# Performance work log

Measured on AMD Instinct MI355X. Metric: run time of the kernel, lower is better.

Reference implementation:

```python
import jax, jax.numpy as jnp
import numpy as np
import math

D_MODEL = 1024
D_K = 256
B, T = 4, 4096

def setup_inputs() -> dict:
    key = jax.random.key(0)
    ks = jax.random.split(key, 7)
    s = 1.0 / math.sqrt(D_MODEL)
    return {
        "inputs": jax.random.normal(ks[0], (B, T, D_MODEL), dtype=jnp.float32),
        "Wq": jax.random.uniform(ks[1], (D_MODEL, D_K), jnp.float32, -s, s),
        "bq": jax.random.uniform(ks[2], (D_K,), jnp.float32, -s, s),
        "Wk": jax.random.uniform(ks[3], (D_MODEL, D_K), jnp.float32, -s, s),
        "bk": jax.random.uniform(ks[4], (D_K,), jnp.float32, -s, s),
        "Wv": jax.random.uniform(ks[5], (D_MODEL, D_K), jnp.float32, -s, s),
        "bv": jax.random.uniform(ks[6], (D_K,), jnp.float32, -s, s),
    }

def reference(inputs, Wq, bq, Wk, bk, Wv, bv):
    q = inputs @ Wq + bq                      # [B,T,d_k]
    k = inputs @ Wk + bk
    v = inputs @ Wv + bv
    scores = jnp.einsum('btd,bsd->bts', q, k)  # [B,T,T]
    Tdim = inputs.shape[1]
    causal = jnp.tril(jnp.ones((Tdim, Tdim), dtype=bool))
    # faithful to original: mask with -1e9 BEFORE dividing by sqrt(d_k)
    scores = jnp.where(causal[None], scores, jnp.float32(-1e9))
    attn = jax.nn.softmax(scores / math.sqrt(D_K), axis=-1)
    return jnp.einsum('bts,bsd->btd', attn, v)
```

## Files before the change

kernel.cpp:

```cpp
#include <hip/hip_runtime.h>
#include <stdint.h>

typedef uint16_t u16;
typedef uint32_t u32;
typedef float    f32x4  __attribute__((ext_vector_type(4)));
typedef short    bf16x8 __attribute__((ext_vector_type(8)));
typedef u32      u32x4  __attribute__((ext_vector_type(4)));
typedef u16      u16x8  __attribute__((ext_vector_type(8)));
typedef u16      u16x4  __attribute__((ext_vector_type(4)));

#define MFMA16(a, b, c) __builtin_amdgcn_mfma_f32_16x16x32_bf16((a), (b), (c), 0, 0, 0)


__device__ __forceinline__ u16 f2bf(float f) {
  u32 x = __float_as_uint(f);
  return (u16)((x + 0x7FFFu + ((x >> 16) & 1u)) >> 16);
}

__global__ __launch_bounds__(256) void cvt_w_kernel(const float* __restrict__ Wq,
                                                    const float* __restrict__ Wk,
                                                    const float* __restrict__ Wv,
                                                    u16* __restrict__ Wt) {
  int idx = blockIdx.x * 256 + threadIdx.x;
  int m = idx >> 18;
  int n = (idx >> 10) & 255;
  int k = idx & 1023;
  const float* W = (m == 0) ? Wq : (m == 1) ? Wk : Wv;
  Wt[idx] = f2bf(W[k * 256 + n]);
}

__global__ __launch_bounds__(256) void qkv_gemm_kernel(
    const float* __restrict__ X, const u16* __restrict__ Wt,
    const float* __restrict__ bq, const float* __restrict__ bk, const float* __restrict__ bv,
    u16* __restrict__ Qb, u16* __restrict__ Kb, u16* __restrict__ Vtb) {
  __shared__ __align__(16) char sm[32768];
  const int tid = threadIdx.x;
  const int wid = tid >> 6, lane = tid & 63, g = lane >> 4, lr = lane & 15;
  const int wr = wid >> 1, wc = wid & 1;
  const int m0 = blockIdx.x * 128, n0 = blockIdx.y * 128, z = blockIdx.z;
  const u16* W = Wt + z * 262144;

  f32x4 acc[4][4];
#pragma unroll
  for (int mi = 0; mi < 4; ++mi)
#pragma unroll
    for (int ni = 0; ni < 4; ++ni) {
      acc[mi][ni][0] = 0.f; acc[mi][ni][1] = 0.f; acc[mi][ni][2] = 0.f; acc[mi][ni][3] = 0.f;
    }

  for (int k0 = 0; k0 < 1024; k0 += 64) {
    __syncthreads();
#pragma unroll
    for (int r = 0; r < 4; ++r) {
      int ch = r * 256 + tid;
      int row = ch >> 3, c = ch & 7;
      const float* xp = X + (size_t)(m0 + row) * 1024 + k0 + c * 8;
      f32x4 xa = *(const f32x4*)xp;
      f32x4 xb = *(const f32x4*)(xp + 4);
      u16x8 xc;
      xc[0] = f2bf(xa[0]); xc[1] = f2bf(xa[1]); xc[2] = f2bf(xa[2]); xc[3] = f2bf(xa[3]);
      xc[4] = f2bf(xb[0]); xc[5] = f2bf(xb[1]); xc[6] = f2bf(xb[2]); xc[7] = f2bf(xb[3]);
      *(u16x8*)(sm + row * 128 + 16 * (c ^ (row & 7))) = xc;
      u32x4 vw = *(const u32x4*)(W + (size_t)(n0 + row) * 1024 + k0 + c * 8);
      *(u32x4*)(sm + 16384 + row * 128 + 16 * (c ^ (row & 7))) = vw;
    }
    __syncthreads();
#pragma unroll
    for (int kk = 0; kk < 2; ++kk) {
      bf16x8 af[4], bfr[4];
#pragma unroll
      for (int mi = 0; mi < 4; ++mi) {
        int row = wr * 64 + mi * 16 + lr;
        af[mi] = *(const bf16x8*)(sm + row * 128 + 16 * ((kk * 4 + g) ^ (row & 7)));
      }
#pragma unroll
      for (int ni = 0; ni < 4; ++ni) {
        int row = wc * 64 + ni * 16 + lr;
        bfr[ni] = *(const bf16x8*)(sm + 16384 + row * 128 + 16 * ((kk * 4 + g) ^ (row & 7)));
      }
#pragma unroll
      for (int mi = 0; mi < 4; ++mi)
#pragma unroll
        for (int ni = 0; ni < 4; ++ni)
          acc[mi][ni] = MFMA16(af[mi], bfr[ni], acc[mi][ni]);
    }
  }

  const float* bias = (z == 0) ? bq : (z == 1) ? bk : bv;
  if (z < 2) {
    u16* O = (z == 0) ? Qb : Kb;
    const float qscale = (z == 0) ? 0.0625f : 1.0f;
#pragma unroll
    for (int ni = 0; ni < 4; ++ni) {
      int col = n0 + wc * 64 + ni * 16 + lr;
      float bb = bias[col];
#pragma unroll
      for (int mi = 0; mi < 4; ++mi)
#pragma unroll
        for (int j = 0; j < 4; ++j) {
          int row = m0 + wr * 64 + mi * 16 + 4 * g + j;
          O[(size_t)row * 256 + col] = f2bf((acc[mi][ni][j] + bb) * qscale);
        }
    }
  } else {
    __syncthreads();
#pragma unroll
    for (int ni = 0; ni < 4; ++ni) {
      int cl = wc * 64 + ni * 16 + lr;
      float bb = bias[n0 + cl];
#pragma unroll
      for (int mi = 0; mi < 4; ++mi)
#pragma unroll
        for (int j = 0; j < 4; ++j) {
          int rl = wr * 64 + mi * 16 + 4 * g + j;
          *(u16*)(sm + cl * 256 + rl * 2) = f2bf(acc[mi][ni][j] + bb);
        }
    }
    __syncthreads();
    int bidx = m0 >> 12, tb = m0 & 4095;
#pragma unroll
    for (int r = 0; r < 8; ++r) {
      int ch = r * 256 + tid;
      int cl = ch >> 4, tp = ch & 15;
      u32x4 v = *(const u32x4*)(sm + cl * 256 + tp * 16);
      *(u32x4*)(Vtb + (size_t)bidx * 1048576 + (size_t)(n0 + cl) * 4096 + tb + tp * 8) = v;
    }
  }
}

__global__ __launch_bounds__(512) void flash_kernel(
    const u16* __restrict__ Qb, const u16* __restrict__ Kb,
    const u16* __restrict__ Vtb, u16* __restrict__ Opart, float2* __restrict__ ML,
    int s, int gx) {
  __shared__ __align__(16) char sm[73728];
  const int tid = threadIdx.x, wid = tid >> 6, lane = tid & 63, g = lane >> 4, lr = lane & 15;
  const int xcd = blockIdx.x & 7;
  const int b = xcd >> 1;
  const int i = ((blockIdx.x >> 3) << 1) + (xcd & 1);
  const int QG = 1 << (s - 1);
  const int NG = 32 >> (s - 1);
  int g4 = 0;
  while (g4 < NG - 1 && i >= (((g4 + 1) * (g4 + 2)) << (s - 2))) ++g4;
  const int local = i - ((g4 * (g4 + 1)) << (s - 2));
  const int qq = local / (g4 + 1);
  const int sc = local - qq * (g4 + 1);
  const int qb = g4 * QG + qq;
  const int t0 = qb * 128;
  const int w0 = t0 + wid * 16;
  const int C = 64 << s;
  const int sbase = sc * C;

  bf16x8 qf[8];
  const u16* Qrow = Qb + (size_t)(b * 4096 + w0 + lr) * 256;
#pragma unroll
  for (int kk = 0; kk < 8; ++kk) qf[kk] = *(const bf16x8*)(Qrow + kk * 32 + g * 8);

  f32x4 o[16];
#pragma unroll
  for (int n = 0; n < 16; ++n) { o[n][0] = 0.f; o[n][1] = 0.f; o[n][2] = 0.f; o[n][3] = 0.f; }
  float m_ = -1e30f, l_ = 0.f;

  const u16* Kbase = Kb + (size_t)b * 4096 * 256;
  const u16* Vbase = Vtb + (size_t)b * 1048576;

  u32x4 pk[4], pv[4];
#define LOADTILE(os_)                                                                      \
  {                                                                                        \
    _Pragma("unroll")                                                                      \
    for (int q = 0; q < 4; ++q) {                                                          \
      int half = q >> 1, rr = q & 1;                                                       \
      int ch = rr * 512 + tid;                          \
      int srow = ch >> 5, c = ch & 31;                                                     \
      pk[q] = *(const u32x4*)(Kbase + (size_t)((os_) + half * 32 + srow) * 256 + c * 8);   \
      int d = ch >> 2, c2 = ch & 3;                                                        \
      pv[q] = *(const u32x4*)(Vbase + (size_t)d * 4096 + (os_) + half * 32 + c2 * 8);      \
    }                                                                                      \
  }

  const int nto = min(C >> 6, (t0 + 128 - sbase) >> 6);
  LOADTILE(sbase);

  for (int ot = 0; ot < nto; ++ot) {
    const int os0 = sbase + ot * 64;
    __syncthreads();
#pragma unroll
    for (int q = 0; q < 4; ++q) {
      int half = q >> 1, rr = q & 1;
      int ch = rr * 512 + tid;
      int srow = ch >> 5, c = ch & 31;
      *(u32x4*)(sm + half * 16384 + srow * 512 + 16 * (c ^ (srow & 7))) = pk[q];
      int d = ch >> 2, c2 = ch & 3;
      *(u32x4*)(sm + 32768 + half * 16384 + d * 64 + 16 * (c2 ^ ((d >> 1) & 3))) = pv[q];
    }
    if (ot + 1 < nto) LOADTILE(os0 + 64);
    __syncthreads();

#pragma unroll 1
    for (int half = 0; half < 2; ++half) {
      const int s0 = os0 + 32 * half;
      if (s0 > w0 + 15) break;
      const char* kb = sm + half * 16384;
      const char* vb = sm + 32768 + half * 16384;

      f32x4 sa[2];
#pragma unroll
      for (int ni = 0; ni < 2; ++ni) { sa[ni][0] = 0.f; sa[ni][1] = 0.f; sa[ni][2] = 0.f; sa[ni][3] = 0.f; }
#pragma unroll
      for (int ni = 0; ni < 2; ++ni) {
        int srw = ni * 16 + lr;
#pragma unroll
        for (int kk = 0; kk < 8; ++kk) {
          bf16x8 kf = *(const bf16x8*)(kb + srw * 512 + 16 * ((kk * 4 + g) ^ (srw & 7)));
          sa[ni] = MFMA16(kf, qf[kk], sa[ni]);
        }
      }
      const int t = w0 + lr;
      if (s0 + 31 > w0) {
#pragma unroll
        for (int ni = 0; ni < 2; ++ni)
#pragma unroll
          for (int j = 0; j < 4; ++j) {
            int ss = s0 + ni * 16 + 4 * g + j;
            if (t < ss) sa[ni][j] = -1e30f;
          }
      }
      float mt = fmaxf(fmaxf(fmaxf(sa[0][0], sa[0][1]), fmaxf(sa[0][2], sa[0][3])),
                       fmaxf(fmaxf(sa[1][0], sa[1][1]), fmaxf(sa[1][2], sa[1][3])));
      mt = fmaxf(mt, __shfl_xor(mt, 16, 64));
      mt = fmaxf(mt, __shfl_xor(mt, 32, 64));
      if (__any(mt > m_ + 8.0f)) {
        float mn = fmaxf(m_, mt);
        float scale = __expf(m_ - mn);
        m_ = mn;
        l_ *= scale;
#pragma unroll
        for (int n = 0; n < 16; ++n)
#pragma unroll
          for (int j = 0; j < 4; ++j) o[n][j] *= scale;
      }
#pragma unroll
      for (int ni = 0; ni < 2; ++ni)
#pragma unroll
        for (int j = 0; j < 4; ++j) sa[ni][j] = __expf(sa[ni][j] - m_);
      float su = (sa[0][0] + sa[0][1]) + (sa[0][2] + sa[0][3]) +
                 (sa[1][0] + sa[1][1]) + (sa[1][2] + sa[1][3]);
      su += __shfl_xor(su, 16, 64);
      su += __shfl_xor(su, 32, 64);
      l_ += su;
#pragma unroll
      for (int ni = 0; ni < 2; ++ni)
#pragma unroll
        for (int j = 0; j < 4; ++j) {
          int c = ni * 2 + (g >> 1);
          *(u16*)(sm + 65536 + wid * 1024 + lr * 64 + 16 * (c ^ (lr & 3)) + (4 * (g & 1) + j) * 2) =
              f2bf(sa[ni][j]);
        }
      asm volatile("s_waitcnt lgkmcnt(0)" ::: "memory");
      bf16x8 pf = *(const bf16x8*)(sm + 65536 + wid * 1024 + lr * 64 + 16 * (g ^ (lr & 3)));
#pragma unroll
      for (int n = 0; n < 16; ++n) {
        int d = n * 16 + lr;
        bf16x8 vf = *(const bf16x8*)(vb + d * 64 + 16 * (g ^ ((d >> 1) & 3)));
        o[n] = MFMA16(vf, pf, o[n]);
      }
    }
  }
#undef LOADTILE

  u16* Orow = Opart + ((size_t)(b * gx + i) * 128 + wid * 16) * 256;
#pragma unroll
  for (int n = 0; n < 16; ++n) {
    u16x4 pkk;
    pkk[0] = f2bf(o[n][0]); pkk[1] = f2bf(o[n][1]); pkk[2] = f2bf(o[n][2]); pkk[3] = f2bf(o[n][3]);
    *(u16x4*)(Orow + lr * 256 + n * 16 + 4 * g) = pkk;
  }
  if (lane < 16) {
    float2 ml; ml.x = m_; ml.y = l_;
    ML[(size_t)(b * gx + i) * 128 + wid * 16 + lane] = ml;
  }
}

__global__ __launch_bounds__(256) void combine_kernel(const u16* __restrict__ Opart,
                                                      const float2* __restrict__ ML,
                                                      float* __restrict__ out,
                                                      int s, int gx) {
  const int wid = threadIdx.x >> 6, lane = threadIdx.x & 63;
  const int rg = blockIdx.x * 4 + wid;
  const int b = rg >> 12, t = rg & 4095;
  const int qb = t >> 7;
  const int gg = qb >> (s - 1), qq = qb & ((1 << (s - 1)) - 1);
  const int n = gg + 1;
  const size_t base = (size_t)(b * gx) + ((gg * (gg + 1)) << (s - 2)) + qq * (gg + 1);
  const int tl = t & 127;
  float mv[8], lv[8], w[8];
  float M = -1e30f;
#pragma unroll
  for (int sc = 0; sc < 8; ++sc)
    if (sc < n) {
      float2 ml = ML[(base + sc) * 128 + tl];
      mv[sc] = ml.x; lv[sc] = ml.y;
      M = fmaxf(M, ml.x);
    }
  float L = 0.f;
#pragma unroll
  for (int sc = 0; sc < 8; ++sc)
    if (sc < n) { w[sc] = __expf(mv[sc] - M); L += w[sc] * lv[sc]; }
  const float inv = 1.0f / L;
  const int c0 = lane * 4;
  float a0 = 0.f, a1 = 0.f, a2 = 0.f, a3 = 0.f;
#pragma unroll
  for (int sc = 0; sc < 8; ++sc)
    if (sc < n) {
      u16x4 v = *(const u16x4*)(Opart + ((base + sc) * 128 + tl) * 256 + c0);
      a0 += w[sc] * __uint_as_float((u32)v[0] << 16);
      a1 += w[sc] * __uint_as_float((u32)v[1] << 16);
      a2 += w[sc] * __uint_as_float((u32)v[2] << 16);
      a3 += w[sc] * __uint_as_float((u32)v[3] << 16);
    }
  f32x4 r; r[0] = a0 * inv; r[1] = a1 * inv; r[2] = a2 * inv; r[3] = a3 * inv;
  *(f32x4*)(out + (size_t)rg * 256 + c0) = r;
}

extern "C" void kernel_launch(void* const* d_in, const int* in_sizes, int n_in,
                              void* d_out, int out_size, void* d_ws, size_t ws_size,
                              hipStream_t stream) {
  const float* X  = (const float*)d_in[0];
  const float* Wq = (const float*)d_in[1];
  const float* bq = (const float*)d_in[2];
  const float* Wk = (const float*)d_in[3];
  const float* bk = (const float*)d_in[4];
  const float* Wv = (const float*)d_in[5];
  const float* bv = (const float*)d_in[6];
  float* out = (float*)d_out;
  char* ws = (char*)d_ws;

  const size_t OFF_WT  = 33554432;
  const size_t OFF_Q   = OFF_WT + 1572864;
  const size_t OFF_K   = OFF_Q + 8388608;
  const size_t OFF_VT  = OFF_K + 8388608;
  const size_t PREFIX  = OFF_VT + 8388608;

  const size_t NEEDED_A = PREFIX + 589824 + 37748736;
  const size_t NEEDED_B = PREFIX + 327680;
  if (ws_size < NEEDED_B) return;

  u16* Wt  = (u16*)(ws + OFF_WT);
  u16* Qb  = (u16*)(ws + OFF_Q);
  u16* Kb  = (u16*)(ws + OFF_K);
  u16* Vtb = (u16*)(ws + OFF_VT);

  int s, gx;
  u16* Opart;
  float2* ML;
  if (ws_size >= NEEDED_A) {
    s = 3; gx = 144;
    ML = (float2*)(ws + PREFIX);
    Opart = (u16*)(ws + PREFIX + 589824);
  } else {
    s = 4; gx = 80;
    ML = (float2*)(ws + PREFIX);
    Opart = (u16*)ws;
  }

  cvt_w_kernel<<<3072, 256, 0, stream>>>(Wq, Wk, Wv, Wt);
  qkv_gemm_kernel<<<dim3(128, 2, 3), 256, 0, stream>>>(X, Wt, bq, bk, bv, Qb, Kb, Vtb);
  flash_kernel<<<4 * gx, 512, 0, stream>>>(Qb, Kb, Vtb, Opart, ML, s, gx);
  combine_kernel<<<4096, 256, 0, stream>>>(Opart, ML, out, s, gx);
}
```

Before: 168.1 us.

## Widen QKV GEMM tile to full 256 columns and reorder flash work items

The QKV projection kernel now uses 512-thread blocks, each covering all 256 output columns for a 128-row slab. Each X tile is therefore loaded and converted to bf16 once instead of twice, at the cost of 64KB of shared memory per block. Separately, the flash kernel's work-item mapping is reordered so that the off-diagonal chunks are scheduled first and the diagonal chunks last, in reverse query order. The combine kernel's indexing is updated to match, which may improve load balance across the causal split.

```diff
diff --git a/kernel.cpp b/kernel.cpp
--- a/kernel.cpp
+++ b/kernel.cpp
@@ -29,15 +29,15 @@
   Wt[idx] = f2bf(W[k * 256 + n]);
 }
 
-__global__ __launch_bounds__(256) void qkv_gemm_kernel(
+__global__ __launch_bounds__(512) void qkv_gemm_kernel(
     const float* __restrict__ X, const u16* __restrict__ Wt,
     const float* __restrict__ bq, const float* __restrict__ bk, const float* __restrict__ bv,
     u16* __restrict__ Qb, u16* __restrict__ Kb, u16* __restrict__ Vtb) {
-  __shared__ __align__(16) char sm[32768];
+  __shared__ __align__(16) char sm[65536];
   const int tid = threadIdx.x;
   const int wid = tid >> 6, lane = tid & 63, g = lane >> 4, lr = lane & 15;
-  const int wr = wid >> 1, wc = wid & 1;
-  const int m0 = blockIdx.x * 128, n0 = blockIdx.y * 128, z = blockIdx.z;
+  const int wr = wid >> 2, wc = wid & 3;
+  const int m0 = blockIdx.x * 128, z = blockIdx.y;
   const u16* W = Wt + z * 262144;
 
   f32x4 acc[4][4];
@@ -51,8 +51,8 @@
   for (int k0 = 0; k0 < 1024; k0 += 64) {
     __syncthreads();
 #pragma unroll
-    for (int r = 0; r < 4; ++r) {
-      int ch = r * 256 + tid;
+    for (int r = 0; r < 2; ++r) {
+      int ch = r * 512 + tid;
       int row = ch >> 3, c = ch & 7;
       const float* xp = X + (size_t)(m0 + row) * 1024 + k0 + c * 8;
       f32x4 xa = *(const f32x4*)xp;
@@ -61,7 +61,12 @@
       xc[0] = f2bf(xa[0]); xc[1] = f2bf(xa[1]); xc[2] = f2bf(xa[2]); xc[3] = f2bf(xa[3]);
       xc[4] = f2bf(xb[0]); xc[5] = f2bf(xb[1]); xc[6] = f2bf(xb[2]); xc[7] = f2bf(xb[3]);
       *(u16x8*)(sm + row * 128 + 16 * (c ^ (row & 7))) = xc;
-      u32x4 vw = *(const u32x4*)(W + (size_t)(n0 + row) * 1024 + k0 + c * 8);
+    }
+#pragma unroll
+    for (int r = 0; r < 4; ++r) {
+      int ch = r * 512 + tid;
+      int row = ch >> 3, c = ch & 7;
+      u32x4 vw = *(const u32x4*)(W + (size_t)row * 1024 + k0 + c * 8);
       *(u32x4*)(sm + 16384 + row * 128 + 16 * (c ^ (row & 7))) = vw;
     }
     __syncthreads();
@@ -92,7 +97,7 @@
     const float qscale = (z == 0) ? 0.0625f : 1.0f;
 #pragma unroll
     for (int ni = 0; ni < 4; ++ni) {
-      int col = n0 + wc * 64 + ni * 16 + lr;
+      int col = wc * 64 + ni * 16 + lr;
       float bb = bias[col];
 #pragma unroll
       for (int mi = 0; mi < 4; ++mi)
@@ -107,7 +112,7 @@
 #pragma unroll
     for (int ni = 0; ni < 4; ++ni) {
       int cl = wc * 64 + ni * 16 + lr;
-      float bb = bias[n0 + cl];
+      float bb = bias[cl];
 #pragma unroll
       for (int mi = 0; mi < 4; ++mi)
 #pragma unroll
@@ -120,10 +125,10 @@
     int bidx = m0 >> 12, tb = m0 & 4095;
 #pragma unroll
     for (int r = 0; r < 8; ++r) {
-      int ch = r * 256 + tid;
+      int ch = r * 512 + tid;
       int cl = ch >> 4, tp = ch & 15;
       u32x4 v = *(const u32x4*)(sm + cl * 256 + tp * 16);
-      *(u32x4*)(Vtb + (size_t)bidx * 1048576 + (size_t)(n0 + cl) * 4096 + tb + tp * 8) = v;
+      *(u32x4*)(Vtb + (size_t)bidx * 1048576 + (size_t)cl * 4096 + tb + tp * 8) = v;
     }
   }
 }
@@ -139,12 +144,22 @@
   const int i = ((blockIdx.x >> 3) << 1) + (xcd & 1);
   const int QG = 1 << (s - 1);
   const int NG = 32 >> (s - 1);
-  int g4 = 0;
-  while (g4 < NG - 1 && i >= (((g4 + 1) * (g4 + 2)) << (s - 2))) ++g4;
-  const int local = i - ((g4 * (g4 + 1)) << (s - 2));
-  const int qq = local / (g4 + 1);
-  const int sc = local - qq * (g4 + 1);
-  const int qb = g4 * QG + qq;
+  const int ND = (QG * NG * (NG - 1)) >> 1;
+  int gg, qq, sc;
+  if (i < ND) {
+    gg = 1;
+    while (gg < NG - 1 && i >= ((QG * (gg + 1) * gg) >> 1)) ++gg;
+    int local = i - ((QG * gg * (gg - 1)) >> 1);
+    qq = local / gg;
+    sc = local - qq * gg;
+  } else {
+    int j = i - ND;
+    int jd = j / NG;
+    qq = (QG - 1) - jd;
+    gg = j - jd * NG;
+    sc = gg;
+  }
+  const int qb = gg * QG + qq;
   const int t0 = qb * 128;
   const int w0 = t0 + wid * 16;
   const int C = 64 << s;
@@ -288,16 +303,21 @@
   const int rg = blockIdx.x * 4 + wid;
   const int b = rg >> 12, t = rg & 4095;
   const int qb = t >> 7;
-  const int gg = qb >> (s - 1), qq = qb & ((1 << (s - 1)) - 1);
+  const int QG = 1 << (s - 1), NG = 32 >> (s - 1);
+  const int ND = (QG * NG * (NG - 1)) >> 1;
+  const int gg = qb >> (s - 1), qq = qb & (QG - 1);
   const int n = gg + 1;
-  const size_t base = (size_t)(b * gx) + ((gg * (gg + 1)) << (s - 2)) + qq * (gg + 1);
+  const int ibase = ((QG * gg * (gg - 1)) >> 1) + qq * gg;
+  const int idiag = ND + (QG - 1 - qq) * NG + gg;
   const int tl = t & 127;
+  int sl[8];
   float mv[8], lv[8], w[8];
   float M = -1e30f;
 #pragma unroll
   for (int sc = 0; sc < 8; ++sc)
     if (sc < n) {
-      float2 ml = ML[(base + sc) * 128 + tl];
+      sl[sc] = b * gx + ((sc < gg) ? (ibase + sc) : idiag);
+      float2 ml = ML[(size_t)sl[sc] * 128 + tl];
       mv[sc] = ml.x; lv[sc] = ml.y;
       M = fmaxf(M, ml.x);
     }
@@ -311,7 +331,7 @@
 #pragma unroll
   for (int sc = 0; sc < 8; ++sc)
     if (sc < n) {
-      u16x4 v = *(const u16x4*)(Opart + ((base + sc) * 128 + tl) * 256 + c0);
+      u16x4 v = *(const u16x4*)(Opart + ((size_t)sl[sc] * 128 + tl) * 256 + c0);
       a0 += w[sc] * __uint_as_float((u32)v[0] << 16);
       a1 += w[sc] * __uint_as_float((u32)v[1] << 16);
       a2 += w[sc] * __uint_as_float((u32)v[2] << 16);
@@ -363,7 +383,7 @@
   }
 
   cvt_w_kernel<<<3072, 256, 0, stream>>>(Wq, Wk, Wv, Wt);
-  qkv_gemm_kernel<<<dim3(128, 2, 3), 256, 0, stream>>>(X, Wt, bq, bk, bv, Qb, Kb, Vtb);
+  qkv_gemm_kernel<<<dim3(128, 3), 512, 0, stream>>>(X, Wt, bq, bk, bv, Qb, Kb, Vtb);
   flash_kernel<<<4 * gx, 512, 0, stream>>>(Qb, Kb, Vtb, Opart, ML, s, gx);
   combine_kernel<<<4096, 256, 0, stream>>>(Opart, ML, out, s, gx);
 }
```

After: 159.8 us. 4.9% less time.
